# Kernel optimization log

Measured on AMD Instinct MI355X. Metric: run time of the kernel, lower is better.

Reference implementation:

```python
import jax, jax.numpy as jnp
import numpy as np

N = 100000      # nodes
E = 1600000     # edges
F_IN = 256      # input features
HID = 64        # hidden channels
C = 10          # classes
EPS = 0.3       # FAGCN epsilon (raw-feature residual scale)
NUM_LAYERS = 2


def setup_inputs() -> dict:
    key = jax.random.key(0)
    ks = jax.random.split(key, 8)
    x = jax.random.normal(ks[0], (N, F_IN), dtype=jnp.float32)
    edge_index = jax.random.randint(ks[1], (2, E), 0, N, dtype=jnp.int32)
    # lin1 / lin2 (xavier-normal-ish scale)
    w1 = jax.random.normal(ks[2], (HID, F_IN), dtype=jnp.float32) * (1.414 / np.sqrt(F_IN))
    b1 = jnp.zeros((HID,), dtype=jnp.float32)
    w2 = jax.random.normal(ks[3], (C, HID), dtype=jnp.float32) * (1.414 / np.sqrt(HID))
    b2 = jnp.zeros((C,), dtype=jnp.float32)
    # per-layer FAConv attention vectors att_l, att_r: [NUM_LAYERS, HID]
    att_l = jax.random.normal(ks[4], (NUM_LAYERS, HID), dtype=jnp.float32) * (1.0 / np.sqrt(HID))
    att_r = jax.random.normal(ks[5], (NUM_LAYERS, HID), dtype=jnp.float32) * (1.0 / np.sqrt(HID))
    return {"x": x, "edge_index": edge_index, "w1": w1, "b1": b1,
            "w2": w2, "b2": b2, "att_l": att_l, "att_r": att_r}


def reference(x, edge_index, w1, b1, w2, b2, att_l, att_r):
    src = edge_index[0]  # [E] message source j
    dst = edge_index[1]  # [E] aggregation target i

    # gcn_norm without self-loops: deg from destination, symmetric normalization
    deg = jax.ops.segment_sum(jnp.ones((E,), x.dtype), dst, num_segments=N)
    dis = jnp.where(deg > 0, jax.lax.rsqrt(jnp.maximum(deg, 1.0)), 0.0)
    norm = dis[src] * dis[dst]  # [E]

    h = jax.nn.relu(x @ w1.T + b1)  # [N, HID]
    raw = h
    for l in range(NUM_LAYERS):
        al = h @ att_l[l]  # [N] per-node left score
        ar = h @ att_r[l]  # [N] per-node right score
        # alpha_j (att_l at source) + alpha_i (att_r at destination)
        alpha = jnp.tanh(al[src] + ar[dst])  # [E]
        msg = h[src] * (alpha * norm)[:, None]  # [E, HID]
        agg = jax.ops.segment_sum(msg, dst, num_segments=N)  # [N, HID]
        h = agg + EPS * raw

    logits = h @ w2.T + b2  # [N, C]
    return jax.nn.log_softmax(logits, axis=1)
```

## Files before the change

kernel.cpp:

```cpp
#include <hip/hip_runtime.h>

#define NN 100000
#define NE 1600000
#define FIN 256
#define HID 64
#define NCLS 10
#define EPSF 0.3f


__global__ void k_wt(const float* __restrict__ w1, float* __restrict__ w1T) {
    int t = blockIdx.x * 256 + threadIdx.x;
    if (t < HID * FIN) {
        int k = t >> 6;
        int h = t & 63;
        w1T[t] = w1[h * FIN + k];
    }
}

__global__ void k_deg(const int* __restrict__ ei, int* __restrict__ deg) {
    int e = blockIdx.x * 256 + threadIdx.x;
    if (e < NE) atomicAdd(&deg[ei[NE + e]], 1);
}

__global__ void k_dis(const int* __restrict__ deg, float* __restrict__ dis) {
    int i = blockIdx.x * 256 + threadIdx.x;
    if (i < NN) {
        int d = deg[i];
        dis[i] = (d > 0) ? (1.0f / sqrtf((float)d)) : 0.0f;
    }
}

__global__ void k_scan1(const int* __restrict__ deg, int* __restrict__ rp, int* __restrict__ bsum) {
    __shared__ int s[1024];
    int i = blockIdx.x * 1024 + threadIdx.x;
    int v = (i < NN) ? deg[i] : 0;
    s[threadIdx.x] = v;
    __syncthreads();
    for (int off = 1; off < 1024; off <<= 1) {
        int t = (threadIdx.x >= off) ? s[threadIdx.x - off] : 0;
        __syncthreads();
        s[threadIdx.x] += t;
        __syncthreads();
    }
    if (i < NN) rp[i] = s[threadIdx.x] - v;
    if (threadIdx.x == 1023) bsum[blockIdx.x] = s[1023];
}

__global__ void k_scan2(int* __restrict__ bsum, int nb) {
    __shared__ int s[128];
    int v = (threadIdx.x < nb) ? bsum[threadIdx.x] : 0;
    s[threadIdx.x] = v;
    __syncthreads();
    for (int off = 1; off < 128; off <<= 1) {
        int t = (threadIdx.x >= off) ? s[threadIdx.x - off] : 0;
        __syncthreads();
        s[threadIdx.x] += t;
        __syncthreads();
    }
    if (threadIdx.x < nb) bsum[threadIdx.x] = s[threadIdx.x] - v;
}

__global__ void k_scan3(int* __restrict__ rp, const int* __restrict__ bsum) {
    int i = blockIdx.x * 1024 + threadIdx.x;
    if (i < NN) rp[i] += bsum[blockIdx.x];
    if (i == 0) rp[NN] = NE;
}

__global__ void k_fill(const int* __restrict__ ei, const int* __restrict__ rp,
                       int* __restrict__ cursor, int* __restrict__ csr_src) {
    int e = blockIdx.x * 256 + threadIdx.x;
    if (e < NE) {
        int s = ei[e], d = ei[NE + e];
        int pos = rp[d] + atomicAdd(&cursor[d], 1);
        csr_src[pos] = s;
    }
}


__global__ __launch_bounds__(256) void k_gemm1(const float* __restrict__ x, const float* __restrict__ w1T,
                                               const float* __restrict__ b1, const float* __restrict__ dis,
                                               const float* __restrict__ att_l0, const float* __restrict__ att_r0,
                                               float* __restrict__ h,
                                               float2* __restrict__ aldis, float2* __restrict__ ardis) {
    __shared__ float4 wlds[FIN * (HID / 4)];
    const float4* __restrict__ wr = reinterpret_cast<const float4*>(w1T);
    for (int t = threadIdx.x; t < FIN * (HID / 4); t += 256) wlds[t] = wr[t];
    __syncthreads();

    int n = blockIdx.x * 256 + threadIdx.x;
    bool act = (n < NN);
    int nc = act ? n : (NN - 1);
    float acc[HID];
#pragma unroll
    for (int j = 0; j < HID; j++) acc[j] = b1[j];
    const float4* __restrict__ xr = reinterpret_cast<const float4*>(x + (size_t)nc * FIN);

    float4 cur = xr[0];
#pragma unroll 1
    for (int k4 = 0; k4 < FIN / 4; k4++) {
        float4 nxt = make_float4(0.f, 0.f, 0.f, 0.f);
        if (k4 < FIN / 4 - 1) nxt = xr[k4 + 1];
        const float* xf = &cur.x;
#pragma unroll
        for (int kk = 0; kk < 4; kk++) {
            float xs = xf[kk];
            const float4* wrow = &wlds[(k4 * 4 + kk) * (HID / 4)];
#pragma unroll
            for (int hq = 0; hq < HID / 4; hq++) {
                float4 wq = wrow[hq];
                acc[hq * 4 + 0] = fmaf(xs, wq.x, acc[hq * 4 + 0]);
                acc[hq * 4 + 1] = fmaf(xs, wq.y, acc[hq * 4 + 1]);
                acc[hq * 4 + 2] = fmaf(xs, wq.z, acc[hq * 4 + 2]);
                acc[hq * 4 + 3] = fmaf(xs, wq.w, acc[hq * 4 + 3]);
            }
        }
        cur = nxt;
    }

    if (!act) return;
    float4* __restrict__ ho = reinterpret_cast<float4*>(h + (size_t)n * HID);
    float p = 0.0f, q = 0.0f;
#pragma unroll
    for (int hq = 0; hq < HID / 4; hq++) {
        float4 v;
        v.x = fmaxf(acc[hq * 4 + 0], 0.0f);
        v.y = fmaxf(acc[hq * 4 + 1], 0.0f);
        v.z = fmaxf(acc[hq * 4 + 2], 0.0f);
        v.w = fmaxf(acc[hq * 4 + 3], 0.0f);
        ho[hq] = v;
        p = fmaf(v.x, att_l0[hq * 4 + 0], p); q = fmaf(v.x, att_r0[hq * 4 + 0], q);
        p = fmaf(v.y, att_l0[hq * 4 + 1], p); q = fmaf(v.y, att_r0[hq * 4 + 1], q);
        p = fmaf(v.z, att_l0[hq * 4 + 2], p); q = fmaf(v.z, att_r0[hq * 4 + 2], q);
        p = fmaf(v.w, att_l0[hq * 4 + 3], p); q = fmaf(v.w, att_r0[hq * 4 + 3], q);
    }
    float ds = dis[n];
    aldis[n] = make_float2(p, ds);
    ardis[n] = make_float2(q, ds);
}

template <int MODE>
__global__ __launch_bounds__(256) void k_agg(const float* __restrict__ h_in, const float* __restrict__ raw,
                                             const int* __restrict__ rp, const int* __restrict__ csr_src,
                                             const float2* __restrict__ aldis_i, const float2* __restrict__ ardis_i,
                                             float* __restrict__ h_out,
                                             const float* __restrict__ att_l, const float* __restrict__ att_r,
                                             const float* __restrict__ dis,
                                             float2* __restrict__ aldis_o, float2* __restrict__ ardis_o,
                                             const float* __restrict__ w2, const float* __restrict__ b2,
                                             float* __restrict__ out) {
    int lane = threadIdx.x & 63;
    int g = lane >> 4;
    int f = lane & 15;
    int i = blockIdx.x * 4 + (threadIdx.x >> 6);
    if (i >= NN) return;
    float2 ai = ardis_i[i];
    int e0 = rp[i], e1 = rp[i + 1];
    int deg = e1 - e0;

    float4 accA = make_float4(0.f, 0.f, 0.f, 0.f);
    float4 accB = make_float4(0.f, 0.f, 0.f, 0.f);

    for (int base = 0; base < deg; base += 64) {
        int rem = deg - base; if (rem > 64) rem = 64;
        int j = 0; float cf = 0.0f;
        if (lane < rem) {
            j = csr_src[e0 + base + lane];
            float2 aj = aldis_i[j];
            cf = tanhf(aj.x + ai.x) * (aj.y * ai.y);
        }
        for (int t = 0; t < rem; t += 8) {
            int i0 = t + g;
            int i1 = t + 4 + g;
            int s0 = i0 < rem ? i0 : rem - 1;
            int s1 = i1 < rem ? i1 : rem - 1;
            int j0 = __shfl(j, s0, 64);
            int j1 = __shfl(j, s1, 64);
            float c0 = __shfl(cf, s0, 64);
            float c1 = __shfl(cf, s1, 64);
            if (i0 >= rem) c0 = 0.0f;
            if (i1 >= rem) c1 = 0.0f;
            float4 h0 = *reinterpret_cast<const float4*>(h_in + j0 * HID + 4 * f);
            float4 h1 = *reinterpret_cast<const float4*>(h_in + j1 * HID + 4 * f);
            accA.x = fmaf(h0.x, c0, accA.x);
            accA.y = fmaf(h0.y, c0, accA.y);
            accA.z = fmaf(h0.z, c0, accA.z);
            accA.w = fmaf(h0.w, c0, accA.w);
            accB.x = fmaf(h1.x, c1, accB.x);
            accB.y = fmaf(h1.y, c1, accB.y);
            accB.z = fmaf(h1.z, c1, accB.z);
            accB.w = fmaf(h1.w, c1, accB.w);
        }
    }
    float4 acc;
    acc.x = accA.x + accB.x;
    acc.y = accA.y + accB.y;
    acc.z = accA.z + accB.z;
    acc.w = accA.w + accB.w;
#pragma unroll
    for (int m = 16; m <= 32; m <<= 1) {
        acc.x += __shfl_xor(acc.x, m, 64);
        acc.y += __shfl_xor(acc.y, m, 64);
        acc.z += __shfl_xor(acc.z, m, 64);
        acc.w += __shfl_xor(acc.w, m, 64);
    }
    float4 rawv = *reinterpret_cast<const float4*>(raw + (size_t)i * HID + 4 * f);
    acc.x = fmaf(EPSF, rawv.x, acc.x);
    acc.y = fmaf(EPSF, rawv.y, acc.y);
    acc.z = fmaf(EPSF, rawv.z, acc.z);
    acc.w = fmaf(EPSF, rawv.w, acc.w);

    if (MODE == 2) {
        float lg[NCLS];
#pragma unroll
        for (int cc = 0; cc < NCLS; cc++) {
            float4 wv = *reinterpret_cast<const float4*>(w2 + cc * HID + 4 * f);
            float p = acc.x * wv.x + acc.y * wv.y + acc.z * wv.z + acc.w * wv.w;
#pragma unroll
            for (int m = 1; m < 16; m <<= 1) p += __shfl_xor(p, m, 64);
            lg[cc] = p + b2[cc];
        }
        float mx = lg[0];
#pragma unroll
        for (int cc = 1; cc < NCLS; cc++) mx = fmaxf(mx, lg[cc]);
        float ssum = 0.0f;
#pragma unroll
        for (int cc = 0; cc < NCLS; cc++) ssum += expf(lg[cc] - mx);
        float r = mx + logf(ssum);
        if (lane < NCLS) {
            float v = 0.0f;
#pragma unroll
            for (int cc = 0; cc < NCLS; cc++)
                if (lane == cc) v = lg[cc];
            out[(size_t)i * NCLS + lane] = v - r;
        }
    } else {
        if (g == 0) *reinterpret_cast<float4*>(h_out + (size_t)i * HID + 4 * f) = acc;
        if (MODE == 1) {
            float4 alv = *reinterpret_cast<const float4*>(att_l + 4 * f);
            float4 arv = *reinterpret_cast<const float4*>(att_r + 4 * f);
            float p = acc.x * alv.x + acc.y * alv.y + acc.z * alv.z + acc.w * alv.w;
            float q = acc.x * arv.x + acc.y * arv.y + acc.z * arv.z + acc.w * arv.w;
#pragma unroll
            for (int m = 1; m < 16; m <<= 1) {
                p += __shfl_xor(p, m, 64);
                q += __shfl_xor(q, m, 64);
            }
            if (lane == 0) {
                float ds = dis[i];
                aldis_o[i] = make_float2(p, ds);
                ardis_o[i] = make_float2(q, ds);
            }
        }
    }
}


extern "C" void kernel_launch(void* const* d_in, const int* in_sizes, int n_in,
                              void* d_out, int out_size, void* d_ws, size_t ws_size,
                              hipStream_t stream) {
    const float* x     = (const float*)d_in[0];
    const int*   ei    = (const int*)d_in[1];
    const float* w1    = (const float*)d_in[2];
    const float* b1    = (const float*)d_in[3];
    const float* w2    = (const float*)d_in[4];
    const float* b2    = (const float*)d_in[5];
    const float* att_l = (const float*)d_in[6];
    const float* att_r = (const float*)d_in[7];
    float* out = (float*)d_out;

    char* ws = (char*)d_ws;
    size_t off = 0;
    auto take = [&](size_t bytes) -> void* {
        void* p = ws + off;
        off += (bytes + 255) & ~(size_t)255;
        return p;
    };
    int*    deg     = (int*)take((size_t)NN * 4);
    int*    cursor  = (int*)take((size_t)NN * 4);
    int*    rp      = (int*)take((size_t)(NN + 1) * 4);
    int*    bsum    = (int*)take(128 * 4);
    float*  dis     = (float*)take((size_t)NN * 4);
    float2* aldisA  = (float2*)take((size_t)NN * 8);
    float2* ardisA  = (float2*)take((size_t)NN * 8);
    float2* aldisB  = (float2*)take((size_t)NN * 8);
    float2* ardisB  = (float2*)take((size_t)NN * 8);
    float*  w1T     = (float*)take((size_t)HID * FIN * 4);
    int*    csr_src = (int*)take((size_t)NE * 4);
    float*  hA      = (float*)take((size_t)NN * HID * 4);
    float*  hB      = (float*)take((size_t)NN * HID * 4);

    hipMemsetAsync(deg, 0, (size_t)NN * 4, stream);
    hipMemsetAsync(cursor, 0, (size_t)NN * 4, stream);

    const int EB = (NE + 255) / 256;
    const int NB = (NN + 255) / 256;
    const int SB = (NN + 1023) / 1024;

    k_wt<<<64, 256, 0, stream>>>(w1, w1T);
    k_deg<<<EB, 256, 0, stream>>>(ei, deg);
    k_dis<<<NB, 256, 0, stream>>>(deg, dis);
    k_scan1<<<SB, 1024, 0, stream>>>(deg, rp, bsum);
    k_scan2<<<1, 128, 0, stream>>>(bsum, SB);
    k_scan3<<<SB, 1024, 0, stream>>>(rp, bsum);
    k_fill<<<EB, 256, 0, stream>>>(ei, rp, cursor, csr_src);

    k_gemm1<<<(NN + 255) / 256, 256, 0, stream>>>(x, w1T, b1, dis, att_l, att_r, hA, aldisA, ardisA);

    k_agg<1><<<NN / 4, 256, 0, stream>>>(hA, hA, rp, csr_src, aldisA, ardisA, hB,
                                         att_l + HID, att_r + HID, dis, aldisB, ardisB,
                                         nullptr, nullptr, nullptr);

    k_agg<2><<<NN / 4, 256, 0, stream>>>(hB, hA, rp, csr_src, aldisB, ardisB, nullptr,
                                         nullptr, nullptr, nullptr, nullptr, nullptr,
                                         w2, b2, out);
}
```

Measured before the change: 536.9 us.

## Use split-fp16 MFMA for lin1 GEMM and bucketed CSR construction

Replaces the scalar FP32 lin1 GEMM with an MFMA kernel that emulates FP32 by splitting x and w1 into fp16 hi/lo parts (three MFMAs per tile), staging x in swizzled LDS. The attention dot products move into a separate k_alar kernel. CSR construction now buckets edges by destination block of 128 nodes, then counts degrees and places sources with LDS atomics instead of global atomics. This trades extra passes and a fixed bucket capacity (BCAP 4096, excess edges silently dropped) for fewer global atomics and much faster matrix math. Precision is reduced slightly, since the lo*lo term is dropped and x below fp16 range loses bits.

```diff
diff --git a/kernel.cpp b/kernel.cpp
--- a/kernel.cpp
+++ b/kernel.cpp
@@ -6,20 +6,50 @@
 #define HID 64
 #define NCLS 10
 #define EPSF 0.3f
-
-
-__global__ void k_wt(const float* __restrict__ w1, float* __restrict__ w1T) {
+#define NBUCK 782
+#define BCAP 4096
+
+typedef _Float16 f16;
+typedef __attribute__((ext_vector_type(4))) _Float16 f16x4;
+typedef __attribute__((ext_vector_type(8))) _Float16 f16x8;
+typedef __attribute__((ext_vector_type(4))) float f32x4;
+
+
+__global__ void k_wt(const float* __restrict__ w1, f16* __restrict__ w_hi, f16* __restrict__ w_lo) {
     int t = blockIdx.x * 256 + threadIdx.x;
     if (t < HID * FIN) {
-        int k = t >> 6;
-        int h = t & 63;
-        w1T[t] = w1[h * FIN + k];
-    }
-}
-
-__global__ void k_deg(const int* __restrict__ ei, int* __restrict__ deg) {
+        float v = w1[t];
+        f16 hi = (f16)v;
+        f16 lo = (f16)(v - (float)hi);
+        w_hi[t] = hi;
+        w_lo[t] = lo;
+    }
+}
+
+__global__ void k_bucket(const int* __restrict__ ei, int* __restrict__ bcnt, int2* __restrict__ bucket) {
     int e = blockIdx.x * 256 + threadIdx.x;
-    if (e < NE) atomicAdd(&deg[ei[NE + e]], 1);
+    if (e < NE) {
+        int s = ei[e], d = ei[NE + e];
+        int b = d >> 7;
+        int p = atomicAdd(&bcnt[b], 1);
+        if (p < BCAP) bucket[b * BCAP + p] = make_int2(s, d);
+    }
+}
+
+__global__ __launch_bounds__(256) void k_cnt(const int* __restrict__ bcnt, const int2* __restrict__ bucket,
+                                             int* __restrict__ deg) {
+    __shared__ int cnt[128];
+    int b = blockIdx.x;
+    if (threadIdx.x < 128) cnt[threadIdx.x] = 0;
+    __syncthreads();
+    int n = bcnt[b]; if (n > BCAP) n = BCAP;
+    for (int t = threadIdx.x; t < n; t += 256)
+        atomicAdd(&cnt[bucket[b * BCAP + t].y & 127], 1);
+    __syncthreads();
+    if (threadIdx.x < 128) {
+        int node = b * 128 + threadIdx.x;
+        if (node < NN) deg[node] = cnt[threadIdx.x];
+    }
 }
 
 __global__ void k_dis(const int* __restrict__ deg, float* __restrict__ dis) {
@@ -66,76 +96,107 @@
     if (i == 0) rp[NN] = NE;
 }
 
-__global__ void k_fill(const int* __restrict__ ei, const int* __restrict__ rp,
-                       int* __restrict__ cursor, int* __restrict__ csr_src) {
-    int e = blockIdx.x * 256 + threadIdx.x;
-    if (e < NE) {
-        int s = ei[e], d = ei[NE + e];
-        int pos = rp[d] + atomicAdd(&cursor[d], 1);
-        csr_src[pos] = s;
-    }
-}
-
-
-__global__ __launch_bounds__(256) void k_gemm1(const float* __restrict__ x, const float* __restrict__ w1T,
-                                               const float* __restrict__ b1, const float* __restrict__ dis,
-                                               const float* __restrict__ att_l0, const float* __restrict__ att_r0,
-                                               float* __restrict__ h,
-                                               float2* __restrict__ aldis, float2* __restrict__ ardis) {
-    __shared__ float4 wlds[FIN * (HID / 4)];
-    const float4* __restrict__ wr = reinterpret_cast<const float4*>(w1T);
-    for (int t = threadIdx.x; t < FIN * (HID / 4); t += 256) wlds[t] = wr[t];
-    __syncthreads();
-
-    int n = blockIdx.x * 256 + threadIdx.x;
-    bool act = (n < NN);
-    int nc = act ? n : (NN - 1);
-    float acc[HID];
-#pragma unroll
-    for (int j = 0; j < HID; j++) acc[j] = b1[j];
-    const float4* __restrict__ xr = reinterpret_cast<const float4*>(x + (size_t)nc * FIN);
-
-    float4 cur = xr[0];
-#pragma unroll 1
-    for (int k4 = 0; k4 < FIN / 4; k4++) {
-        float4 nxt = make_float4(0.f, 0.f, 0.f, 0.f);
-        if (k4 < FIN / 4 - 1) nxt = xr[k4 + 1];
-        const float* xf = &cur.x;
-#pragma unroll
-        for (int kk = 0; kk < 4; kk++) {
-            float xs = xf[kk];
-            const float4* wrow = &wlds[(k4 * 4 + kk) * (HID / 4)];
-#pragma unroll
-            for (int hq = 0; hq < HID / 4; hq++) {
-                float4 wq = wrow[hq];
-                acc[hq * 4 + 0] = fmaf(xs, wq.x, acc[hq * 4 + 0]);
-                acc[hq * 4 + 1] = fmaf(xs, wq.y, acc[hq * 4 + 1]);
-                acc[hq * 4 + 2] = fmaf(xs, wq.z, acc[hq * 4 + 2]);
-                acc[hq * 4 + 3] = fmaf(xs, wq.w, acc[hq * 4 + 3]);
+__global__ __launch_bounds__(256) void k_place(const int* __restrict__ bcnt, const int2* __restrict__ bucket,
+                                               const int* __restrict__ rp, int* __restrict__ csr_src) {
+    __shared__ int cur[128];
+    int b = blockIdx.x;
+    if (threadIdx.x < 128) cur[threadIdx.x] = 0;
+    __syncthreads();
+    int n = bcnt[b]; if (n > BCAP) n = BCAP;
+    for (int t = threadIdx.x; t < n; t += 256) {
+        int2 sd = bucket[b * BCAP + t];
+        int p = rp[sd.y] + atomicAdd(&cur[sd.y & 127], 1);
+        csr_src[p] = sd.x;
+    }
+}
+
+
+__global__ __launch_bounds__(256) void k_gemm1(const float* __restrict__ x,
+                                               const f16* __restrict__ w_hi, const f16* __restrict__ w_lo,
+                                               const float* __restrict__ b1, float* __restrict__ h) {
+    __shared__ f16 Ah[64 * 256];
+    __shared__ f16 Al[64 * 256];
+    int tid = threadIdx.x;
+    int m0 = blockIdx.x * 64;
+
+#pragma unroll
+    for (int it = 0; it < 16; ++it) {
+        int flat4 = it * 256 + tid;
+        int row = flat4 >> 6;
+        int col4 = flat4 & 63;
+        int grow = m0 + row; if (grow >= NN) grow = NN - 1;
+        float4 xv = *reinterpret_cast<const float4*>(x + (size_t)grow * FIN + col4 * 4);
+        f16x4 hi, lo;
+        hi[0] = (f16)xv.x; lo[0] = (f16)(xv.x - (float)hi[0]);
+        hi[1] = (f16)xv.y; lo[1] = (f16)(xv.y - (float)hi[1]);
+        hi[2] = (f16)xv.z; lo[2] = (f16)(xv.z - (float)hi[2]);
+        hi[3] = (f16)xv.w; lo[3] = (f16)(xv.w - (float)hi[3]);
+        int hb = (col4 * 4) ^ ((row & 7) << 3);
+        *reinterpret_cast<f16x4*>(&Ah[row * 256 + hb]) = hi;
+        *reinterpret_cast<f16x4*>(&Al[row * 256 + hb]) = lo;
+    }
+    __syncthreads();
+
+    int lane = tid & 63;
+    int wave = tid >> 6;
+    int lg = lane >> 4;
+    int lr = lane & 15;
+    int arow = wave * 16 + lr;
+
+    f32x4 acc[4];
+#pragma unroll
+    for (int nt = 0; nt < 4; ++nt) acc[nt] = (f32x4){0.f, 0.f, 0.f, 0.f};
+
+#pragma unroll
+    for (int kt = 0; kt < 8; ++kt) {
+        int kb = kt * 32 + lg * 8;
+        int ha = arow * 256 + (kb ^ ((arow & 7) << 3));
+        f16x8 a_hi = *reinterpret_cast<const f16x8*>(&Ah[ha]);
+        f16x8 a_lo = *reinterpret_cast<const f16x8*>(&Al[ha]);
+#pragma unroll
+        for (int nt = 0; nt < 4; ++nt) {
+            int bidx = (nt * 16 + lr) * 256 + kb;
+            f16x8 b_hi = *reinterpret_cast<const f16x8*>(&w_hi[bidx]);
+            f16x8 b_lo = *reinterpret_cast<const f16x8*>(&w_lo[bidx]);
+            acc[nt] = __builtin_amdgcn_mfma_f32_16x16x32_f16(a_hi, b_hi, acc[nt], 0, 0, 0);
+            acc[nt] = __builtin_amdgcn_mfma_f32_16x16x32_f16(a_lo, b_hi, acc[nt], 0, 0, 0);
+            acc[nt] = __builtin_amdgcn_mfma_f32_16x16x32_f16(a_hi, b_lo, acc[nt], 0, 0, 0);
+        }
+    }
+
+#pragma unroll
+    for (int nt = 0; nt < 4; ++nt) {
+        int col = nt * 16 + lr;
+        float bb = b1[col];
+#pragma unroll
+        for (int r = 0; r < 4; ++r) {
+            int node = m0 + wave * 16 + lg * 4 + r;
+            if (node < NN) {
+                float v = fmaxf(acc[nt][r] + bb, 0.0f);
+                h[(size_t)node * HID + col] = v;
             }
         }
-        cur = nxt;
-    }
-
-    if (!act) return;
-    float4* __restrict__ ho = reinterpret_cast<float4*>(h + (size_t)n * HID);
-    float p = 0.0f, q = 0.0f;
-#pragma unroll
-    for (int hq = 0; hq < HID / 4; hq++) {
-        float4 v;
-        v.x = fmaxf(acc[hq * 4 + 0], 0.0f);
-        v.y = fmaxf(acc[hq * 4 + 1], 0.0f);
-        v.z = fmaxf(acc[hq * 4 + 2], 0.0f);
-        v.w = fmaxf(acc[hq * 4 + 3], 0.0f);
-        ho[hq] = v;
-        p = fmaf(v.x, att_l0[hq * 4 + 0], p); q = fmaf(v.x, att_r0[hq * 4 + 0], q);
-        p = fmaf(v.y, att_l0[hq * 4 + 1], p); q = fmaf(v.y, att_r0[hq * 4 + 1], q);
-        p = fmaf(v.z, att_l0[hq * 4 + 2], p); q = fmaf(v.z, att_r0[hq * 4 + 2], q);
-        p = fmaf(v.w, att_l0[hq * 4 + 3], p); q = fmaf(v.w, att_r0[hq * 4 + 3], q);
-    }
-    float ds = dis[n];
-    aldis[n] = make_float2(p, ds);
-    ardis[n] = make_float2(q, ds);
+    }
+}
+
+__global__ void k_alar(const float* __restrict__ h, const float* __restrict__ att_l, const float* __restrict__ att_r,
+                       const float* __restrict__ dis, float2* __restrict__ aldis, float2* __restrict__ ardis) {
+    int lane = threadIdx.x & 63;
+    int i = blockIdx.x * 4 + (threadIdx.x >> 6);
+    if (i >= NN) return;
+    float hv = h[(size_t)i * HID + lane];
+    float p = hv * att_l[lane];
+    float q = hv * att_r[lane];
+#pragma unroll
+    for (int m = 1; m < 64; m <<= 1) {
+        p += __shfl_xor(p, m, 64);
+        q += __shfl_xor(q, m, 64);
+    }
+    if (lane == 0) {
+        float ds = dis[i];
+        aldis[i] = make_float2(p, ds);
+        ardis[i] = make_float2(q, ds);
+    }
 }
 
 template <int MODE>
@@ -276,35 +337,38 @@
         return p;
     };
     int*    deg     = (int*)take((size_t)NN * 4);
-    int*    cursor  = (int*)take((size_t)NN * 4);
     int*    rp      = (int*)take((size_t)(NN + 1) * 4);
     int*    bsum    = (int*)take(128 * 4);
+    int*    bcnt    = (int*)take((size_t)NBUCK * 4);
     float*  dis     = (float*)take((size_t)NN * 4);
     float2* aldisA  = (float2*)take((size_t)NN * 8);
     float2* ardisA  = (float2*)take((size_t)NN * 8);
     float2* aldisB  = (float2*)take((size_t)NN * 8);
     float2* ardisB  = (float2*)take((size_t)NN * 8);
-    float*  w1T     = (float*)take((size_t)HID * FIN * 4);
+    f16*    w_hi    = (f16*)take((size_t)HID * FIN * 2);
+    f16*    w_lo    = (f16*)take((size_t)HID * FIN * 2);
+    int2*   bucket  = (int2*)take((size_t)NBUCK * BCAP * 8);
     int*    csr_src = (int*)take((size_t)NE * 4);
     float*  hA      = (float*)take((size_t)NN * HID * 4);
     float*  hB      = (float*)take((size_t)NN * HID * 4);
 
-    hipMemsetAsync(deg, 0, (size_t)NN * 4, stream);
-    hipMemsetAsync(cursor, 0, (size_t)NN * 4, stream);
+    hipMemsetAsync(bcnt, 0, (size_t)NBUCK * 4, stream);
 
     const int EB = (NE + 255) / 256;
     const int NB = (NN + 255) / 256;
     const int SB = (NN + 1023) / 1024;
 
-    k_wt<<<64, 256, 0, stream>>>(w1, w1T);
-    k_deg<<<EB, 256, 0, stream>>>(ei, deg);
+    k_wt<<<64, 256, 0, stream>>>(w1, w_hi, w_lo);
+    k_bucket<<<EB, 256, 0, stream>>>(ei, bcnt, bucket);
+    k_cnt<<<NBUCK, 256, 0, stream>>>(bcnt, bucket, deg);
     k_dis<<<NB, 256, 0, stream>>>(deg, dis);
     k_scan1<<<SB, 1024, 0, stream>>>(deg, rp, bsum);
     k_scan2<<<1, 128, 0, stream>>>(bsum, SB);
     k_scan3<<<SB, 1024, 0, stream>>>(rp, bsum);
-    k_fill<<<EB, 256, 0, stream>>>(ei, rp, cursor, csr_src);
-
-    k_gemm1<<<(NN + 255) / 256, 256, 0, stream>>>(x, w1T, b1, dis, att_l, att_r, hA, aldisA, ardisA);
+    k_place<<<NBUCK, 256, 0, stream>>>(bcnt, bucket, rp, csr_src);
+
+    k_gemm1<<<(NN + 63) / 64, 256, 0, stream>>>(x, w_hi, w_lo, b1, hA);
+    k_alar<<<NN / 4, 256, 0, stream>>>(hA, att_l, att_r, dis, aldisA, ardisA);
 
     k_agg<1><<<NN / 4, 256, 0, stream>>>(hA, hA, rp, csr_src, aldisA, ardisA, hB,
                                          att_l + HID, att_r + HID, dis, aldisB, ardisB,
```

After: 805.0 us. +50.0%, slower.
